# Optimization experiments

Measured on AMD Instinct MI355X. Metric: run time of the kernel, lower is better.

## Reference

```python
import jax, jax.numpy as jnp
import numpy as np

K = 3          # kernel_size
DIL = 2        # dilation
PAD = 2        # unfold padding
EPS = 1e-5     # InstanceNorm eps


def setup_inputs() -> dict:
    key = jax.random.key(0)
    ks = jax.random.split(key, 6)
    b, c, h, w = 8, 128, 128, 128
    c_red = c // 8                      # reduction_ratio = 8
    k2 = K * K
    x = jax.random.normal(ks[0], (b, c, h, w), dtype=jnp.float32)
    # conv1: 1x1, channels -> channels//8, no bias
    w1 = jax.random.normal(ks[1], (c_red, c), dtype=jnp.float32) * (1.0 / np.sqrt(c))
    # InstanceNorm2d affine params
    in_gamma = jnp.ones((c_red,), dtype=jnp.float32)
    in_beta = jnp.zeros((c_red,), dtype=jnp.float32)
    # conv2: 1x1, channels//8 -> k^2 * groups (groups == channels since group_channels=1)
    w2 = jax.random.normal(ks[2], (k2 * c, c_red), dtype=jnp.float32) * (1.0 / np.sqrt(c_red))
    b2 = jnp.zeros((k2 * c,), dtype=jnp.float32)
    return {"x": x, "w1": w1, "in_gamma": in_gamma, "in_beta": in_beta, "w2": w2, "b2": b2}


def reference(x, w1, in_gamma, in_beta, w2, b2):
    b, c, h, w = x.shape
    k2 = K * K
    # --- weight generation branch (stride == 1, ZeroPad2d arg is 0 -> no-op) ---
    t = jnp.einsum('oc,bchw->bohw', w1, x)                      # 1x1 conv, no bias
    mean = t.mean(axis=(2, 3), keepdims=True)                   # InstanceNorm2d (biased var)
    var = t.var(axis=(2, 3), keepdims=True)
    t = (t - mean) * jax.lax.rsqrt(var + EPS)
    t = t * in_gamma[None, :, None, None] + in_beta[None, :, None, None]
    t = jax.nn.relu(t)
    wgt = jnp.einsum('oc,bchw->bohw', w2, t) + b2[None, :, None, None]
    wgt = wgt.reshape(b, c, k2, h, w)                           # (b, groups=c, k^2, h, w)
    # --- unfold: dilated 3x3 patches, padding=2 -> same spatial size ---
    xp = jnp.pad(x, ((0, 0), (0, 0), (PAD, PAD), (PAD, PAD)))
    patches = jnp.stack(
        [xp[:, :, DIL * i:DIL * i + h, DIL * j:DIL * j + w]
         for i in range(K) for j in range(K)], axis=2)          # (b, c, k^2, h, w)
    # --- dynamic-weight multiply + reduce over kernel taps ---
    return (wgt * patches).sum(axis=2)                          # (b, c, h, w)
```

## Files before the change

kernel.cpp:

```cpp
#include <hip/hip_runtime.h>

#define BB   8
#define CC   128
#define CR   16
#define HH   128
#define WW   128
#define HWSZ 16384
#define K2   9
#define NFRAG 72

typedef _Float16 f16x8 __attribute__((ext_vector_type(8)));
typedef float    f32x4 __attribute__((ext_vector_type(4)));

#define WS_T     0
#define WS_PART  2097152
#define WS_TN16  2113792
#define WS_AFRAG 3162368

__global__ __launch_bounds__(256) void k_conv1(const float* __restrict__ x,
                                               const float* __restrict__ w1,
                                               const float* __restrict__ w2,
                                               const float* __restrict__ b2,
                                               float* __restrict__ ws) {
    const int bid = blockIdx.x;
    const int tid = threadIdx.x;

    if (bid >= 512) {
        const int id = (bid - 512) * 256 + tid;
        if (id >= NFRAG * 64) return;
        const int lane = id & 63;
        const int frag = id >> 6;
        const int ct = frag / 9, k = frag - ct * 9;
        const int row = lane & 15, lg = lane >> 4;
        f16x8 v;
#pragma unroll
        for (int i = 0; i < 8; ++i) {
            const int kk = lg * 8 + i;
            float w = 0.f;
            if (kk < CR)        w = w2[(size_t)((ct * 16 + row) * K2 + k) * CR + kk];
            else if (kk == CR)  w = b2[(ct * 16 + row) * K2 + k];
            v[i] = (_Float16)w;
        }
        f16x8* dst = (f16x8*)(ws + WS_AFRAG);
        dst[frag * 64 + lane] = v;
        return;
    }

    const int tile = bid & 63;
    const int b    = bid >> 6;
    const int pix  = tile * 256 + tid;

    __shared__ float w1s[CR * CC];
    for (int i = tid; i < CR * CC; i += 256) w1s[i] = w1[i];
    __syncthreads();

    const float* xb = x + (size_t)b * CC * HWSZ + pix;
    float acc[CR];
#pragma unroll
    for (int o = 0; o < CR; ++o) acc[o] = 0.f;

    for (int cin = 0; cin < CC; ++cin) {
        float xv = xb[(size_t)cin * HWSZ];
#pragma unroll
        for (int o = 0; o < CR; ++o)
            acc[o] = fmaf(w1s[o * CC + cin], xv, acc[o]);
    }

    float* tb = ws + WS_T + (size_t)b * CR * HWSZ + pix;
#pragma unroll
    for (int o = 0; o < CR; ++o) tb[(size_t)o * HWSZ] = acc[o];

    __shared__ float red[4][CR][2];
    const int lane = tid & 63;
    const int wv   = tid >> 6;
#pragma unroll
    for (int o = 0; o < CR; ++o) {
        float s = acc[o];
        float q = s * s;
#pragma unroll
        for (int off = 32; off > 0; off >>= 1) {
            s += __shfl_down(s, off, 64);
            q += __shfl_down(q, off, 64);
        }
        if (lane == 0) { red[wv][o][0] = s; red[wv][o][1] = q; }
    }
    __syncthreads();
    if (tid < CR) {
        const int o = tid;
        float s = red[0][o][0] + red[1][o][0] + red[2][o][0] + red[3][o][0];
        float q = red[0][o][1] + red[1][o][1] + red[2][o][1] + red[3][o][1];
        const int blk = b * 64 + tile;
        float* part = ws + WS_PART;
        part[blk * 32 + o * 2 + 0] = s;
        part[blk * 32 + o * 2 + 1] = q;
    }
}

__global__ __launch_bounds__(256) void k_norm(const float* __restrict__ ws_t,
                                              const float* __restrict__ part,
                                              const float* __restrict__ gamma,
                                              const float* __restrict__ beta,
                                              f16x8* __restrict__ tn16) {
    const int tid = threadIdx.x;
    const int p   = blockIdx.x * 256 + tid;
    const int b   = p >> 14;
    const int pp  = p & 16383;

    __shared__ float sts[CR][2];
    {
        const int o  = tid >> 4;
        const int t4 = tid & 15;
        float s = 0.f, q = 0.f;
        if (o < CR) {
#pragma unroll
            for (int j = 0; j < 4; ++j) {
                const int blk = b * 64 + t4 + j * 16;
                s += part[blk * 32 + o * 2 + 0];
                q += part[blk * 32 + o * 2 + 1];
            }
#pragma unroll
            for (int off = 8; off > 0; off >>= 1) {
                s += __shfl_down(s, off, 16);
                q += __shfl_down(q, off, 16);
            }
            if (t4 == 0) {
                const float mean = s * (1.f / (float)HWSZ);
                const float var  = q * (1.f / (float)HWSZ) - mean * mean;
                const float rstd = rsqrtf(var + 1e-5f);
                const float sc   = gamma[o] * rstd;
                sts[o][0] = sc;
                sts[o][1] = beta[o] - mean * sc;
            }
        }
    }
    __syncthreads();

    const float* tb = ws_t + (size_t)b * CR * HWSZ + pp;
    f16x8 lo, hi;
#pragma unroll
    for (int i = 0; i < 8; ++i) {
        float v0 = fmaf(tb[(size_t)i * HWSZ],       sts[i][0],     sts[i][1]);
        float v1 = fmaf(tb[(size_t)(i + 8) * HWSZ], sts[i + 8][0], sts[i + 8][1]);
        lo[i] = (_Float16)(v0 > 0.f ? v0 : 0.f);
        hi[i] = (_Float16)(v1 > 0.f ? v1 : 0.f);
    }
    tn16[(size_t)p * 2 + 0] = lo;
    tn16[(size_t)p * 2 + 1] = hi;
}

__global__ __launch_bounds__(256) void k_main(const float* __restrict__ x,
                                              const float* __restrict__ ws,
                                              float* __restrict__ out) {
    const int bid = blockIdx.x;
    const int w   = (bid & 7) * 512 + (bid >> 3);
    const int y4    = w & 31;
    const int xhalf = (w >> 5) & 1;
    const int ct    = (w >> 6) & 7;
    const int b     = w >> 9;

    const int tid  = threadIdx.x;
    const int wv   = tid >> 6;
    const int lane = tid & 63;
    const int lg   = lane >> 4;
    const int ln   = lane & 15;
    const int y    = y4 * 4 + wv;

    const f16x8* afr = (const f16x8*)(ws + WS_AFRAG) + (size_t)ct * K2 * 64 + lane;
    f16x8 af[K2];
#pragma unroll
    for (int k = 0; k < K2; ++k) af[k] = afr[k * 64];

    const int crow = lg * 4;
    const int cb   = ct * 16 + crow;
    const float* xp = x   + ((size_t)b * CC + cb) * HWSZ;
    float*       op = out + ((size_t)b * CC + cb) * HWSZ;
    const f16x8* tns = (const f16x8*)(ws + WS_TN16) + ((size_t)b << 15);
    const bool yint = (y >= 2) && (y < HH - 2);
    const f32x4 zc = {0.f, 0.f, 0.f, 0.f};

#pragma unroll 1
    for (int g = 0; g < 4; ++g) {
        const int colb = xhalf * 64 + g * 16;
        const int col  = colb + ln;
        const int pix  = y * WW + col;

        f16x8 tnf = {};
        if (lg < 2) {
            tnf = tns[(size_t)pix * 2 + lg];
        } else if (lg == 2) {
            tnf[0] = (_Float16)1.f;
        }

        f32x4 acc = {0.f, 0.f, 0.f, 0.f};
        const bool xint = (colb >= 2) && (colb + 17 < WW);

        if (yint && xint) {
            const float* q0 = xp + pix;
            const float* q1 = q0 + HWSZ;
            const float* q2 = q0 + 2 * HWSZ;
            const float* q3 = q0 + 3 * HWSZ;
#pragma unroll
            for (int k = 0; k < K2; ++k) {
                const int d = ((k / 3) * 2 - 2) * WW + ((k % 3) * 2 - 2);
                const f32x4 wg = __builtin_amdgcn_mfma_f32_16x16x32_f16(af[k], tnf, zc, 0, 0, 0);
                acc[0] = fmaf(wg[0], q0[d], acc[0]);
                acc[1] = fmaf(wg[1], q1[d], acc[1]);
                acc[2] = fmaf(wg[2], q2[d], acc[2]);
                acc[3] = fmaf(wg[3], q3[d], acc[3]);
            }
        } else {
            int  xoff[3];
            bool xm[3];
#pragma unroll
            for (int j = 0; j < 3; ++j) {
                const int xx = col + (j * 2 - 2);
                xm[j]   = ((unsigned)xx < (unsigned)WW);
                xoff[j] = xx & (WW - 1);
            }
#pragma unroll
            for (int k = 0; k < K2; ++k) {
                const int yy  = y + ((k / 3) * 2 - 2);
                const int off = ((yy & (HH - 1)) << 7) + xoff[k % 3];
                const float m = (xm[k % 3] && ((unsigned)yy < (unsigned)HH)) ? 1.f : 0.f;
                const f32x4 wg = __builtin_amdgcn_mfma_f32_16x16x32_f16(af[k], tnf, zc, 0, 0, 0);
                acc[0] = fmaf(wg[0], xp[off + 0 * HWSZ] * m, acc[0]);
                acc[1] = fmaf(wg[1], xp[off + 1 * HWSZ] * m, acc[1]);
                acc[2] = fmaf(wg[2], xp[off + 2 * HWSZ] * m, acc[2]);
                acc[3] = fmaf(wg[3], xp[off + 3 * HWSZ] * m, acc[3]);
            }
        }

        float* o = op + pix;
        __builtin_nontemporal_store(acc[0], o + 0 * HWSZ);
        __builtin_nontemporal_store(acc[1], o + 1 * HWSZ);
        __builtin_nontemporal_store(acc[2], o + 2 * HWSZ);
        __builtin_nontemporal_store(acc[3], o + 3 * HWSZ);
    }
}

extern "C" void kernel_launch(void* const* d_in, const int* in_sizes, int n_in,
                              void* d_out, int out_size, void* d_ws, size_t ws_size,
                              hipStream_t stream) {
    const float* x     = (const float*)d_in[0];
    const float* w1    = (const float*)d_in[1];
    const float* gamma = (const float*)d_in[2];
    const float* beta  = (const float*)d_in[3];
    const float* w2    = (const float*)d_in[4];
    const float* b2    = (const float*)d_in[5];
    float* out = (float*)d_out;

    float* ws = (float*)d_ws;

    k_conv1<<<530, 256, 0, stream>>>(x, w1, w2, b2, ws);

    k_norm<<<512, 256, 0, stream>>>(ws + WS_T, ws + WS_PART, gamma, beta,
                                    (f16x8*)(ws + WS_TN16));

    k_main<<<4096, 256, 0, stream>>>(x, ws, out);
}
```

Baseline: 72.82 us.

## Store conv1 output as fp16 split planes and prefetch normalized tiles in main

The conv1 kernel now writes its 16-channel intermediate as two fp16 vector planes instead of 16 fp32 planes. This halves that intermediate traffic and lets the norm kernel read it with two vector loads. The normalized activations are also split into separate lo/hi planes so main-kernel loads are contiguous per lane group. The main kernel prefetches the next column group's fragment during the current iteration. Storing pre-norm values in fp16 adds rounding before normalization, which could cost accuracy.

```diff
diff --git a/kernel.cpp b/kernel.cpp
--- a/kernel.cpp
+++ b/kernel.cpp
@@ -12,10 +12,12 @@
 typedef _Float16 f16x8 __attribute__((ext_vector_type(8)));
 typedef float    f32x4 __attribute__((ext_vector_type(4)));
 
-#define WS_T     0
-#define WS_PART  2097152
-#define WS_TN16  2113792
-#define WS_AFRAG 3162368
+#define WS_PART   0
+#define WS_TRAWLO 16384
+#define WS_TRAWHI 540672
+#define WS_TNLO   1064960
+#define WS_TNHI   1589248
+#define WS_AFRAG  2113536
 
 __global__ __launch_bounds__(256) void k_conv1(const float* __restrict__ x,
                                                const float* __restrict__ w1,
@@ -66,9 +68,16 @@
             acc[o] = fmaf(w1s[o * CC + cin], xv, acc[o]);
     }
 
-    float* tb = ws + WS_T + (size_t)b * CR * HWSZ + pix;
-#pragma unroll
-    for (int o = 0; o < CR; ++o) tb[(size_t)o * HWSZ] = acc[o];
+    {
+        f16x8 lo, hi;
+#pragma unroll
+        for (int i = 0; i < 8; ++i) {
+            lo[i] = (_Float16)acc[i];
+            hi[i] = (_Float16)acc[i + 8];
+        }
+        ((f16x8*)(ws + WS_TRAWLO))[(size_t)b * HWSZ + pix] = lo;
+        ((f16x8*)(ws + WS_TRAWHI))[(size_t)b * HWSZ + pix] = hi;
+    }
 
     __shared__ float red[4][CR][2];
     const int lane = tid & 63;
@@ -96,15 +105,15 @@
     }
 }
 
-__global__ __launch_bounds__(256) void k_norm(const float* __restrict__ ws_t,
-                                              const float* __restrict__ part,
+__global__ __launch_bounds__(256) void k_norm(const float* __restrict__ ws_in,
                                               const float* __restrict__ gamma,
                                               const float* __restrict__ beta,
-                                              f16x8* __restrict__ tn16) {
+                                              float* __restrict__ ws_out) {
     const int tid = threadIdx.x;
     const int p   = blockIdx.x * 256 + tid;
     const int b   = p >> 14;
-    const int pp  = p & 16383;
+
+    const float* part = ws_in + WS_PART;
 
     __shared__ float sts[CR][2];
     {
@@ -135,17 +144,18 @@
     }
     __syncthreads();
 
-    const float* tb = ws_t + (size_t)b * CR * HWSZ + pp;
-    f16x8 lo, hi;
+    const f16x8 lo = ((const f16x8*)(ws_in + WS_TRAWLO))[p];
+    const f16x8 hi = ((const f16x8*)(ws_in + WS_TRAWHI))[p];
+    f16x8 nlo, nhi;
 #pragma unroll
     for (int i = 0; i < 8; ++i) {
-        float v0 = fmaf(tb[(size_t)i * HWSZ],       sts[i][0],     sts[i][1]);
-        float v1 = fmaf(tb[(size_t)(i + 8) * HWSZ], sts[i + 8][0], sts[i + 8][1]);
-        lo[i] = (_Float16)(v0 > 0.f ? v0 : 0.f);
-        hi[i] = (_Float16)(v1 > 0.f ? v1 : 0.f);
-    }
-    tn16[(size_t)p * 2 + 0] = lo;
-    tn16[(size_t)p * 2 + 1] = hi;
+        float v0 = fmaf((float)lo[i], sts[i][0],     sts[i][1]);
+        float v1 = fmaf((float)hi[i], sts[i + 8][0], sts[i + 8][1]);
+        nlo[i] = (_Float16)(v0 > 0.f ? v0 : 0.f);
+        nhi[i] = (_Float16)(v1 > 0.f ? v1 : 0.f);
+    }
+    ((f16x8*)(ws_out + WS_TNLO))[p] = nlo;
+    ((f16x8*)(ws_out + WS_TNHI))[p] = nhi;
 }
 
 __global__ __launch_bounds__(256) void k_main(const float* __restrict__ x,
@@ -165,6 +175,14 @@
     const int ln   = lane & 15;
     const int y    = y4 * 4 + wv;
 
+    const f16x8* tp = (const f16x8*)(ws + (lg == 1 ? WS_TNHI : WS_TNLO))
+                      + ((size_t)b << 14);
+    const int tbase = y * WW + xhalf * 64 + ln;
+
+    f16x8 tnf = {}, tnf_nxt = {};
+    if (lg < 2)  tnf = tp[tbase];
+    if (lg == 2) tnf[0] = (_Float16)1.f;
+
     const f16x8* afr = (const f16x8*)(ws + WS_AFRAG) + (size_t)ct * K2 * 64 + lane;
     f16x8 af[K2];
 #pragma unroll
@@ -174,7 +192,6 @@
     const int cb   = ct * 16 + crow;
     const float* xp = x   + ((size_t)b * CC + cb) * HWSZ;
     float*       op = out + ((size_t)b * CC + cb) * HWSZ;
-    const f16x8* tns = (const f16x8*)(ws + WS_TN16) + ((size_t)b << 15);
     const bool yint = (y >= 2) && (y < HH - 2);
     const f32x4 zc = {0.f, 0.f, 0.f, 0.f};
 
@@ -184,12 +201,8 @@
         const int col  = colb + ln;
         const int pix  = y * WW + col;
 
-        f16x8 tnf = {};
-        if (lg < 2) {
-            tnf = tns[(size_t)pix * 2 + lg];
-        } else if (lg == 2) {
-            tnf[0] = (_Float16)1.f;
-        }
+        if (g < 3 && lg < 2)
+            tnf_nxt = tp[tbase + (g + 1) * 16];
 
         f32x4 acc = {0.f, 0.f, 0.f, 0.f};
         const bool xint = (colb >= 2) && (colb + 17 < WW);
@@ -235,6 +248,9 @@
         __builtin_nontemporal_store(acc[1], o + 1 * HWSZ);
         __builtin_nontemporal_store(acc[2], o + 2 * HWSZ);
         __builtin_nontemporal_store(acc[3], o + 3 * HWSZ);
+
+        tnf = tnf_nxt;
+        if (lg == 2) tnf[0] = (_Float16)1.f;
     }
 }
 
@@ -253,8 +269,7 @@
 
     k_conv1<<<530, 256, 0, stream>>>(x, w1, w2, b2, ws);
 
-    k_norm<<<512, 256, 0, stream>>>(ws + WS_T, ws + WS_PART, gamma, beta,
-                                    (f16x8*)(ws + WS_TN16));
+    k_norm<<<512, 256, 0, stream>>>(ws, gamma, beta, ws);
 
     k_main<<<4096, 256, 0, stream>>>(x, ws, out);
 }
```

Result: faster. 70.04 us (-3.8%).
